# Kernel optimization log

Measured on AMD Instinct MI355X. Metric: run time of the kernel, lower is better.

## Reference

```python
import jax, jax.numpy as jnp
import numpy as np

M_ROWS, K, N = 4096, 4096, 4096
DIVFACTOR = 1.0 / (127.0 * 127.0)


def setup_inputs() -> dict:
    key = jax.random.key(0)
    k1, k2, k3, k4, k5 = jax.random.split(key, 5)
    # quantized activations and weights, int8 range
    x = jax.random.randint(k1, (M_ROWS, K), -128, 128, dtype=jnp.int32).astype(jnp.int8)
    scale_x = jnp.abs(jax.random.normal(k2, (M_ROWS,), dtype=jnp.float32)) * 0.01
    weight_int8 = jax.random.randint(k3, (N, K), -128, 128, dtype=jnp.int32).astype(jnp.int8)
    scale_w = jnp.abs(jax.random.normal(k4, (N,), dtype=jnp.float32)) * 0.01
    bias = (jax.random.normal(k5, (N,), dtype=jnp.float32) * 0.01).astype(jnp.float16)
    return {"x": x, "scale_x": scale_x, "weight_int8": weight_int8, "scale_w": scale_w, "bias": bias}


def reference(x, scale_x, weight_int8, scale_w, bias):
    # int8 @ int8^T accumulated (reference path computes in fp32, like torch .float())
    acc = jnp.matmul(x.astype(jnp.float32), weight_int8.T.astype(jnp.float32))  # [M, N]
    out = scale_w[None, :] * (scale_x[:, None] * (acc * DIVFACTOR))
    out = out + bias[None, :].astype(jnp.float32)  # bias promoted fp16->fp32, as in torch
    return out.astype(jnp.float16)
```

## Files before the change

kernel.cpp:

```cpp
#include <hip/hip_runtime.h>
#include <hip/hip_fp16.h>

typedef int v4i __attribute__((ext_vector_type(4)));
typedef const unsigned __attribute__((address_space(1)))* gas_t;
typedef unsigned __attribute__((address_space(3)))* las_t;

#define DIVFACTOR (1.0f / 16129.0f)

__device__ __forceinline__ unsigned pack4(int4 v) {
    return (unsigned)(v.x & 0xFF) | ((unsigned)(v.y & 0xFF) << 8) |
           ((unsigned)(v.z & 0xFF) << 16) | ((unsigned)v.w << 24);
}

__device__ __forceinline__ void gload16(const void* g, void* l) {
    __builtin_amdgcn_global_load_lds((gas_t)g, (las_t)l, 16, 0, 0);
}

__global__ __launch_bounds__(256) void pack_kernel(
    const int* __restrict__ x, const int* __restrict__ w, uint4* __restrict__ ws)
{
    const int u   = blockIdx.x * 256 + threadIdx.x;
    const int g   = u & 3;
    const int row = (u >> 2) & 127;
    const int kt  = (u >> 9) & 63;
    const int p   = u >> 15;
    const int* src = (blockIdx.y == 0) ? x : w;
    uint4* dst = ws + (size_t)blockIdx.y * 1048576;

    const int4* s = (const int4*)(src + (size_t)(p * 128 + row) * 4096 + kt * 64 + g * 16);
    int4 s0 = s[0], s1 = s[1], s2 = s[2], s3 = s[3];
    uint4 d = make_uint4(pack4(s0), pack4(s1), pack4(s2), pack4(s3));
    dst[(((size_t)(p * 64 + kt)) << 9) + row * 4 + g] = d;
}

__global__ __launch_bounds__(256) void i8gemm_packed(
    const uint4* __restrict__ Ap, const uint4* __restrict__ Bp,
    const float* __restrict__ scale_x, const float* __restrict__ scale_w,
    const void* __restrict__ bias, float* __restrict__ out)
{
    __shared__ unsigned lds[8192];

    const int t    = threadIdx.x;
    const int bx   = blockIdx.x;
    const int by   = blockIdx.y;
    const int lane = t & 63;
    const int wid  = t >> 6;
    const int wr   = wid >> 1;
    const int wc   = wid & 1;
    const int r    = lane & 15;
    const int g    = lane >> 4;

    const uint4* aSrc = Ap + (size_t)by * 32768 + t;
    const uint4* bSrc = Bp + (size_t)bx * 32768 + t;
    unsigned* la0 = lds + t * 4;
    unsigned* lb0 = lds + 4096 + t * 4;

    const int a_off = (wr * 64 + r) * 64 + g * 16;
    const int b_off = (wc * 64 + r) * 64 + g * 16;
    const char* ldsc = (const char*)lds;

    v4i acc[4][4];
    #pragma unroll
    for (int m = 0; m < 4; ++m)
        #pragma unroll
        for (int n = 0; n < 4; ++n) acc[m][n] = (v4i){0, 0, 0, 0};

    for (int kt2 = 0; kt2 < 32; ++kt2) {
        __syncthreads();
        #pragma unroll
        for (int sub = 0; sub < 2; ++sub) {
            const uint4* as = aSrc + (size_t)(kt2 * 2 + sub) * 512;
            const uint4* bs = bSrc + (size_t)(kt2 * 2 + sub) * 512;
            gload16(as,       la0 + sub * 2048);
            gload16(as + 256, la0 + sub * 2048 + 1024);
            gload16(bs,       lb0 + sub * 2048);
            gload16(bs + 256, lb0 + sub * 2048 + 1024);
        }
        __syncthreads();

        #pragma unroll
        for (int ks = 0; ks < 2; ++ks) {
            v4i af[4], bf[4];
            #pragma unroll
            for (int m = 0; m < 4; ++m)
                af[m] = *(const v4i*)(ldsc + ks * 8192 + a_off + m * 1024);
            #pragma unroll
            for (int n = 0; n < 4; ++n)
                bf[n] = *(const v4i*)(ldsc + 16384 + ks * 8192 + b_off + n * 1024);
            #pragma unroll
            for (int m = 0; m < 4; ++m)
                #pragma unroll
                for (int n = 0; n < 4; ++n)
                    acc[m][n] = __builtin_amdgcn_mfma_i32_16x16x64_i8(af[m], bf[n], acc[m][n], 0, 0, 0);
        }
    }

    const float p0  = ((const float*)bias)[0];
    const float ap0 = fabsf(p0);
    const bool bias_is_f32 = (ap0 >= 1e-6f && ap0 <= 1.0f);

    float sxv[4][4];
    #pragma unroll
    for (int m = 0; m < 4; ++m)
        #pragma unroll
        for (int q = 0; q < 4; ++q)
            sxv[m][q] = scale_x[by * 128 + wr * 64 + m * 16 + g * 4 + q] * DIVFACTOR;

    float swv[4], bvv[4];
    #pragma unroll
    for (int n = 0; n < 4; ++n) {
        int col = bx * 128 + wc * 64 + n * 16 + r;
        swv[n] = scale_w[col];
        bvv[n] = bias_is_f32 ? ((const float*)bias)[col]
                             : __half2float(((const __half*)bias)[col]);
    }

    #pragma unroll
    for (int m = 0; m < 4; ++m) {
        #pragma unroll
        for (int q = 0; q < 4; ++q) {
            int row = by * 128 + wr * 64 + m * 16 + g * 4 + q;
            float s = sxv[m][q];
            #pragma unroll
            for (int n = 0; n < 4; ++n) {
                int col = bx * 128 + wc * 64 + n * 16 + r;
                float v = (float)acc[m][n][q] * s * swv[n] + bvv[n];
                out[(size_t)row * 4096 + col] = __half2float(__float2half(v));
            }
        }
    }
}

__global__ __launch_bounds__(256) void i8gemm_kernel(
    const int* __restrict__ x, const int* __restrict__ w,
    const float* __restrict__ scale_x, const float* __restrict__ scale_w,
    const void* __restrict__ bias, float* __restrict__ out)
{
    __shared__ int lds[4096];
    const int t = threadIdx.x, bx = blockIdx.x, by = blockIdx.y;
    const int lane = t & 63, wid = t >> 6, wr = wid >> 1, wc = wid & 1;
    const int th = t >> 4, tl = t & 15;
    const int* aptr = x + (size_t)(by * 128 + th) * 4096 + tl * 4;
    const int* bptr = w + (size_t)(bx * 128 + th) * 4096 + tl * 4;
    const int wbase = th * 16 + (tl ^ (((th >> 1) & 3) << 2));
    const int r = lane & 15, g = lane >> 4;
    const int sw4 = (r >> 1) & 3;
    const int a_rd = (wr * 64 + r) * 16 + ((g ^ sw4) << 2);
    const int b_rd = 2048 + (wc * 64 + r) * 16 + ((g ^ sw4) << 2);

    v4i acc[4][4];
    #pragma unroll
    for (int m = 0; m < 4; ++m)
        #pragma unroll
        for (int n = 0; n < 4; ++n) acc[m][n] = (v4i){0, 0, 0, 0};

    int4 va[8], vb[8];
    #pragma unroll
    for (int j = 0; j < 8; ++j) { va[j] = *(const int4*)(aptr + j * 65536); vb[j] = *(const int4*)(bptr + j * 65536); }

    for (int kt = 0; kt < 64; ++kt) {
        __syncthreads();
        #pragma unroll
        for (int j = 0; j < 8; ++j) {
            lds[wbase + j * 256]        = (int)pack4(va[j]);
            lds[2048 + wbase + j * 256] = (int)pack4(vb[j]);
        }
        __syncthreads();
        if (kt < 63) {
            const int* ap = aptr + (kt + 1) * 64;
            const int* bp = bptr + (kt + 1) * 64;
            #pragma unroll
            for (int j = 0; j < 8; ++j) { va[j] = *(const int4*)(ap + j * 65536); vb[j] = *(const int4*)(bp + j * 65536); }
        }
        v4i af[4], bf[4];
        #pragma unroll
        for (int m = 0; m < 4; ++m) af[m] = *(const v4i*)&lds[a_rd + m * 256];
        #pragma unroll
        for (int n = 0; n < 4; ++n) bf[n] = *(const v4i*)&lds[b_rd + n * 256];
        #pragma unroll
        for (int m = 0; m < 4; ++m)
            #pragma unroll
            for (int n = 0; n < 4; ++n)
                acc[m][n] = __builtin_amdgcn_mfma_i32_16x16x64_i8(af[m], bf[n], acc[m][n], 0, 0, 0);
    }

    const float p0 = ((const float*)bias)[0];
    const float ap0 = fabsf(p0);
    const bool bias_is_f32 = (ap0 >= 1e-6f && ap0 <= 1.0f);
    float sxv[4][4];
    #pragma unroll
    for (int m = 0; m < 4; ++m)
        #pragma unroll
        for (int q = 0; q < 4; ++q)
            sxv[m][q] = scale_x[by * 128 + wr * 64 + m * 16 + g * 4 + q] * DIVFACTOR;
    float swv[4], bvv[4];
    #pragma unroll
    for (int n = 0; n < 4; ++n) {
        int col = bx * 128 + wc * 64 + n * 16 + r;
        swv[n] = scale_w[col];
        bvv[n] = bias_is_f32 ? ((const float*)bias)[col] : __half2float(((const __half*)bias)[col]);
    }
    #pragma unroll
    for (int m = 0; m < 4; ++m)
        #pragma unroll
        for (int q = 0; q < 4; ++q) {
            int row = by * 128 + wr * 64 + m * 16 + g * 4 + q;
            float s = sxv[m][q];
            #pragma unroll
            for (int n = 0; n < 4; ++n) {
                int col = bx * 128 + wc * 64 + n * 16 + r;
                float v = (float)acc[m][n][q] * s * swv[n] + bvv[n];
                out[(size_t)row * 4096 + col] = __half2float(__float2half(v));
            }
        }
}

extern "C" void kernel_launch(void* const* d_in, const int* in_sizes, int n_in,
                              void* d_out, int out_size, void* d_ws, size_t ws_size,
                              hipStream_t stream) {
    const int*   x   = (const int*)d_in[0];
    const float* sx  = (const float*)d_in[1];
    const int*   w   = (const int*)d_in[2];
    const float* sw  = (const float*)d_in[3];
    const void*  bi  = d_in[4];
    float*       out = (float*)d_out;
    (void)in_sizes; (void)n_in; (void)out_size;

    if (ws_size >= (size_t)33554432) {
        uint4* ws = (uint4*)d_ws;
        hipLaunchKernelGGL(pack_kernel, dim3(4096, 2, 1), dim3(256, 1, 1), 0, stream, x, w, ws);
        hipLaunchKernelGGL(i8gemm_packed, dim3(32, 32, 1), dim3(256, 1, 1), 0, stream,
                           ws, ws + 1048576, sx, sw, bi, out);
    } else {
        hipLaunchKernelGGL(i8gemm_kernel, dim3(32, 32, 1), dim3(256, 1, 1), 0, stream,
                           x, w, sx, sw, bi, out);
    }
}
```

Before: 255.9 us.

## Rewrite packed int8 GEMM as 256x256 double-buffered 8-phase pipelined kernel

The packed GEMM now uses 256x256 output tiles with 512 threads per block, which halves redundant global loads per output. A double-buffered 128 KB LDS pipeline interleaves global_load_lds staging with MFMA clusters, using explicit s_barrier, vmcnt waits and setprio. The pack kernel writes 128-wide K tiles with an XOR swizzle so LDS fragment reads avoid bank conflicts. A grid remap groups blocks for L2 locality. In exchange the kernel runs one block per CU with high register pressure, and the hand-tuned waits must line up exactly with the load order.

```diff
diff --git a/kernel.cpp b/kernel.cpp
--- a/kernel.cpp
+++ b/kernel.cpp
@@ -20,111 +20,147 @@
     const int* __restrict__ x, const int* __restrict__ w, uint4* __restrict__ ws)
 {
     const int u   = blockIdx.x * 256 + threadIdx.x;
-    const int g   = u & 3;
-    const int row = (u >> 2) & 127;
-    const int kt  = (u >> 9) & 63;
-    const int p   = u >> 15;
+    const int s   = u & 7;
+    const int row = (u >> 3) & 127;
+    const int h   = (u >> 10) & 1;
+    const int kt  = (u >> 11) & 31;
+    const int p   = u >> 16;
     const int* src = (blockIdx.y == 0) ? x : w;
     uint4* dst = ws + (size_t)blockIdx.y * 1048576;
 
-    const int4* s = (const int4*)(src + (size_t)(p * 128 + row) * 4096 + kt * 64 + g * 16);
-    int4 s0 = s[0], s1 = s[1], s2 = s[2], s3 = s[3];
+    const int grow = p * 256 + h * 128 + row;
+    const int4* sp = (const int4*)(src + (size_t)grow * 4096 + kt * 128 + s * 16);
+    int4 s0 = sp[0], s1 = sp[1], s2 = sp[2], s3 = sp[3];
     uint4 d = make_uint4(pack4(s0), pack4(s1), pack4(s2), pack4(s3));
-    dst[(((size_t)(p * 64 + kt)) << 9) + row * 4 + g] = d;
-}
-
-__global__ __launch_bounds__(256) void i8gemm_packed(
+    dst[(((size_t)((p * 32 + kt) * 2 + h)) << 10) + row * 8 + (s ^ (row & 7))] = d;
+}
+
+__global__ __launch_bounds__(512, 1) void i8gemm_8ph(
     const uint4* __restrict__ Ap, const uint4* __restrict__ Bp,
     const float* __restrict__ scale_x, const float* __restrict__ scale_w,
     const void* __restrict__ bias, float* __restrict__ out)
 {
-    __shared__ unsigned lds[8192];
+    __shared__ uint4 ldsq[8192];
+    char* ldsb = (char*)ldsq;
+
+    const int bid = blockIdx.x;
+    const int swb = ((bid & 7) << 5) | (bid >> 3);
+    const int bx  = swb & 15;
+    const int by  = swb >> 4;
 
     const int t    = threadIdx.x;
-    const int bx   = blockIdx.x;
-    const int by   = blockIdx.y;
     const int lane = t & 63;
     const int wid  = t >> 6;
-    const int wr   = wid >> 1;
-    const int wc   = wid & 1;
+    const int wr   = wid >> 2;
+    const int wc   = wid & 3;
     const int r    = lane & 15;
     const int g    = lane >> 4;
 
-    const uint4* aSrc = Ap + (size_t)by * 32768 + t;
-    const uint4* bSrc = Bp + (size_t)bx * 32768 + t;
-    unsigned* la0 = lds + t * 4;
-    unsigned* lb0 = lds + 4096 + t * 4;
-
-    const int a_off = (wr * 64 + r) * 64 + g * 16;
-    const int b_off = (wc * 64 + r) * 64 + g * 16;
-    const char* ldsc = (const char*)lds;
-
-    v4i acc[4][4];
-    #pragma unroll
-    for (int m = 0; m < 4; ++m)
+    const uint4* aBase = Ap + (size_t)by * 65536 + t;
+    const uint4* bBase = Bp + (size_t)bx * 65536 + t;
+
+    const int sl0 = ((g ^ (r & 7)) << 4);
+    const int sl1 = (((4 + g) ^ (r & 7)) << 4);
+    const int aoff0 = wr * 16384 + r * 128 + sl0;
+    const int aoff1 = wr * 16384 + r * 128 + sl1;
+    const int boff0 = 32768 + (wc >> 1) * 16384 + ((wc & 1) * 64 + r) * 128 + sl0;
+    const int boff1 = 32768 + (wc >> 1) * 16384 + ((wc & 1) * 64 + r) * 128 + sl1;
+
+#define ARD(BUF,M,KS) (*(const v4i*)(ldsb + (BUF)*65536 + aoff##KS + (M)*2048))
+#define BRD(BUF,N,KS) (*(const v4i*)(ldsb + (BUF)*65536 + boff##KS + (N)*2048))
+
+#define STAGE(KT, MAT, HALF, BUF) do{ \
+    const uint4* s_ = ((MAT) ? bBase : aBase) + (KT)*2048 + (HALF)*1024; \
+    char* d_ = ldsb + (BUF)*65536 + (MAT)*32768 + (HALF)*16384 + t*16; \
+    gload16((const void*)s_, (void*)d_); \
+    gload16((const void*)(s_ + 512), (void*)(d_ + 8192)); \
+}while(0)
+
+#define BAR asm volatile("s_barrier" ::: "memory")
+
+#define RD_B_A01(BUF) do{ \
+    _Pragma("unroll") for (int n_ = 0; n_ < 4; ++n_) { bfr[n_][0] = BRD(BUF,n_,0); bfr[n_][1] = BRD(BUF,n_,1); } \
+    afr[0][0]=ARD(BUF,0,0); afr[0][1]=ARD(BUF,0,1); afr[1][0]=ARD(BUF,1,0); afr[1][1]=ARD(BUF,1,1); \
+}while(0)
+
+#define RD_A27(BUF) do{ \
+    _Pragma("unroll") for (int m_ = 2; m_ < 8; ++m_) { afr[m_][0] = ARD(BUF,m_,0); afr[m_][1] = ARD(BUF,m_,1); } \
+}while(0)
+
+#define CLUSTER(MA,MB) do{ \
+    __builtin_amdgcn_s_setprio(1); \
+    _Pragma("unroll") for (int n_ = 0; n_ < 4; ++n_) { \
+        acc[MA][n_] = __builtin_amdgcn_mfma_i32_16x16x64_i8(afr[MA][0], bfr[n_][0], acc[MA][n_], 0,0,0); \
+        acc[MA][n_] = __builtin_amdgcn_mfma_i32_16x16x64_i8(afr[MA][1], bfr[n_][1], acc[MA][n_], 0,0,0); \
+        acc[MB][n_] = __builtin_amdgcn_mfma_i32_16x16x64_i8(afr[MB][0], bfr[n_][0], acc[MB][n_], 0,0,0); \
+        acc[MB][n_] = __builtin_amdgcn_mfma_i32_16x16x64_i8(afr[MB][1], bfr[n_][1], acc[MB][n_], 0,0,0); } \
+    __builtin_amdgcn_s_setprio(0); \
+}while(0)
+
+#define ITER(KB, STEADY) do{ \
+    RD_B_A01(0); STAGE((KB)+1,1,0,1); BAR; CLUSTER(0,1); BAR;                  \
+    RD_A27(0);   STAGE((KB)+1,1,1,1); BAR; CLUSTER(2,3); BAR;                  \
+    if (STEADY) STAGE((KB)+2,0,0,0); BAR; CLUSTER(4,5); BAR;                   \
+    if (STEADY) { STAGE((KB)+2,0,1,0); asm volatile("s_waitcnt vmcnt(4)" ::: "memory"); } \
+    else        { asm volatile("s_waitcnt vmcnt(0)" ::: "memory"); } \
+    BAR; CLUSTER(6,7); BAR;                                                    \
+    RD_B_A01(1); if (STEADY) STAGE((KB)+2,1,0,0); BAR; CLUSTER(0,1); BAR;      \
+    RD_A27(1);   if (STEADY) STAGE((KB)+2,1,1,0); BAR; CLUSTER(2,3); BAR;      \
+    if (STEADY) STAGE((KB)+3,0,0,1); BAR; CLUSTER(4,5); BAR;                   \
+    if (STEADY) { STAGE((KB)+3,0,1,1); asm volatile("s_waitcnt vmcnt(4)" ::: "memory"); } \
+    BAR; CLUSTER(6,7); BAR;                                                    \
+}while(0)
+
+    v4i acc[8][4];
+    #pragma unroll
+    for (int m = 0; m < 8; ++m)
         #pragma unroll
         for (int n = 0; n < 4; ++n) acc[m][n] = (v4i){0, 0, 0, 0};
-
-    for (int kt2 = 0; kt2 < 32; ++kt2) {
-        __syncthreads();
-        #pragma unroll
-        for (int sub = 0; sub < 2; ++sub) {
-            const uint4* as = aSrc + (size_t)(kt2 * 2 + sub) * 512;
-            const uint4* bs = bSrc + (size_t)(kt2 * 2 + sub) * 512;
-            gload16(as,       la0 + sub * 2048);
-            gload16(as + 256, la0 + sub * 2048 + 1024);
-            gload16(bs,       lb0 + sub * 2048);
-            gload16(bs + 256, lb0 + sub * 2048 + 1024);
-        }
-        __syncthreads();
-
-        #pragma unroll
-        for (int ks = 0; ks < 2; ++ks) {
-            v4i af[4], bf[4];
-            #pragma unroll
-            for (int m = 0; m < 4; ++m)
-                af[m] = *(const v4i*)(ldsc + ks * 8192 + a_off + m * 1024);
-            #pragma unroll
-            for (int n = 0; n < 4; ++n)
-                bf[n] = *(const v4i*)(ldsc + 16384 + ks * 8192 + b_off + n * 1024);
-            #pragma unroll
-            for (int m = 0; m < 4; ++m)
-                #pragma unroll
-                for (int n = 0; n < 4; ++n)
-                    acc[m][n] = __builtin_amdgcn_mfma_i32_16x16x64_i8(af[m], bf[n], acc[m][n], 0, 0, 0);
-        }
-    }
+    v4i afr[8][2], bfr[4][2];
+
+    STAGE(0,0,0,0); STAGE(0,0,1,0); STAGE(0,1,0,0); STAGE(0,1,1,0);
+    STAGE(1,0,0,1); STAGE(1,0,1,1);
+    asm volatile("s_waitcnt vmcnt(4)" ::: "memory");
+    BAR;
+
+    for (int i = 0; i < 15; ++i) { ITER(2 * i, 1); }
+    ITER(30, 0);
+
+#undef ITER
+#undef CLUSTER
+#undef RD_A27
+#undef RD_B_A01
+#undef BAR
+#undef STAGE
+#undef BRD
+#undef ARD
 
     const float p0  = ((const float*)bias)[0];
     const float ap0 = fabsf(p0);
     const bool bias_is_f32 = (ap0 >= 1e-6f && ap0 <= 1.0f);
 
-    float sxv[4][4];
-    #pragma unroll
-    for (int m = 0; m < 4; ++m)
-        #pragma unroll
-        for (int q = 0; q < 4; ++q)
-            sxv[m][q] = scale_x[by * 128 + wr * 64 + m * 16 + g * 4 + q] * DIVFACTOR;
-
     float swv[4], bvv[4];
     #pragma unroll
     for (int n = 0; n < 4; ++n) {
-        int col = bx * 128 + wc * 64 + n * 16 + r;
+        int col = bx * 256 + wc * 64 + n * 16 + r;
         swv[n] = scale_w[col];
         bvv[n] = bias_is_f32 ? ((const float*)bias)[col]
                              : __half2float(((const __half*)bias)[col]);
     }
 
     #pragma unroll
-    for (int m = 0; m < 4; ++m) {
+    for (int m = 0; m < 8; ++m) {
+        float sxr[4];
+        #pragma unroll
+        for (int q = 0; q < 4; ++q)
+            sxr[q] = scale_x[by * 256 + wr * 128 + m * 16 + g * 4 + q] * DIVFACTOR;
         #pragma unroll
         for (int q = 0; q < 4; ++q) {
-            int row = by * 128 + wr * 64 + m * 16 + g * 4 + q;
-            float s = sxv[m][q];
+            int row = by * 256 + wr * 128 + m * 16 + g * 4 + q;
             #pragma unroll
             for (int n = 0; n < 4; ++n) {
-                int col = bx * 128 + wc * 64 + n * 16 + r;
-                float v = (float)acc[m][n][q] * s * swv[n] + bvv[n];
+                int col = bx * 256 + wc * 64 + n * 16 + r;
+                float v = (float)acc[m][n][q] * sxr[q] * swv[n] + bvv[n];
                 out[(size_t)row * 4096 + col] = __half2float(__float2half(v));
             }
         }
@@ -229,7 +265,7 @@
     if (ws_size >= (size_t)33554432) {
         uint4* ws = (uint4*)d_ws;
         hipLaunchKernelGGL(pack_kernel, dim3(4096, 2, 1), dim3(256, 1, 1), 0, stream, x, w, ws);
-        hipLaunchKernelGGL(i8gemm_packed, dim3(32, 32, 1), dim3(256, 1, 1), 0, stream,
+        hipLaunchKernelGGL(i8gemm_8ph, dim3(256, 1, 1), dim3(512, 1, 1), 0, stream,
                            ws, ws + 1048576, sx, sw, bi, out);
     } else {
         hipLaunchKernelGGL(i8gemm_kernel, dim3(32, 32, 1), dim3(256, 1, 1), 0, stream,
```

Measured after the change: 231.3 us. 9.6% less time.
